# Kernel tuning notes

Hardware: AMD Instinct MI355X
Metric: run time of the kernel (lower is better)

The kernel has to match this reference:

```python
import jax, jax.numpy as jnp
import numpy as np

UNITS = 512
CONN = 512          # input feature dim (connections)
DEND_SIZE = 16
SEQL = CONN // DEND_SIZE  # 32 dendrite segments per unit
BATCH = 512


def _make_dendrites(units, conn, dsize, seed=0):
    # Per-unit random permutation of input indices, grouped into contiguous
    # dendrites of size dsize -> segment id in [0, seql) for every input index.
    rng = np.random.default_rng(seed)
    seql = conn // dsize
    seg = np.empty((units, conn), dtype=np.int32)
    for u in range(units):
        perm = rng.permutation(conn)
        for s in range(seql):
            seg[u, perm[dsize * s:dsize * (s + 1)]] = s
    return seg


def setup_inputs() -> dict:
    key = jax.random.key(0)
    k1, k2, k3, k4 = jax.random.split(key, 4)
    x = jax.random.normal(k1, (BATCH, CONN), dtype=jnp.float32)
    # weight_twice & not uniqueW -> per-unit scalar input weight, shape [1, units]
    kernel = jax.random.uniform(k2, (1, UNITS), dtype=jnp.float32, minval=5e-5, maxval=0.1)
    # per-(segment, unit) dendritic weight, shape [seql, units]
    dendriticW = jax.random.uniform(k3, (SEQL, UNITS), dtype=jnp.float32, minval=5e-5, maxval=0.1)
    bias = jax.random.normal(k4, (UNITS,), dtype=jnp.float32) * 0.05
    dendrites = jnp.asarray(_make_dendrites(UNITS, CONN, DEND_SIZE))  # [units, conn] int32
    return {"x": x, "kernel": kernel, "dendriticW": dendriticW,
            "bias": bias, "dendrites": dendrites}


def reference(x, kernel, dendriticW, bias, dendrites):
    # x: [batch, conn]; dendrites: [units, conn] segment ids in [0, SEQL)
    xT = x.T  # [conn, batch]
    # per-unit gather + unsorted_segment_sum over connections -> [units, seql, batch]
    segsum = jax.vmap(lambda seg: jax.ops.segment_sum(xT, seg, num_segments=SEQL))(dendrites)
    # weight_twice: per-unit scalar input weight (kernel broadcast over conn)
    segsum = segsum * kernel[0][:, None, None]
    # dendritic weighting + reduction over segments -> [batch, units]
    out = jnp.einsum('usb,su->bu', segsum, dendriticW) + bias
    return jax.nn.relu(out)
```

## Files before the change

kernel.cpp:

```cpp
#include <hip/hip_runtime.h>
#include <hip/hip_bf16.h>

#define UNITS 512
#define CONN  512
#define SEQL  32

typedef __hip_bfloat16 bf16;
typedef __attribute__((ext_vector_type(8))) short short8;
typedef __attribute__((ext_vector_type(4))) float floatx4;


union cv8 { bf16 h[8]; short8 v; };

__global__ __launch_bounds__(256) void dendriter_fused_mfma(
    const float* __restrict__ x,
    const float* __restrict__ kern,
    const float* __restrict__ dW,
    const float* __restrict__ bias,
    const int*   __restrict__ dend,
    float* __restrict__ out)
{
    __shared__ short8 wl[16][65];

    const int t  = threadIdx.x;
    const int ut = blockIdx.x * 16;
    const int bt = blockIdx.y * 64;

    {
        const int ul  = t >> 4;
        const int cg0 = (t & 15) * 4;
        const int u   = ut + ul;
        const float kv = kern[u];
        const int4* dp = (const int4*)(dend + u * CONN + cg0 * 8);
#pragma unroll
        for (int j = 0; j < 4; ++j) {
            const int4 s0 = dp[2 * j];
            const int4 s1 = dp[2 * j + 1];
            const int segs[8] = {s0.x, s0.y, s0.z, s0.w, s1.x, s1.y, s1.z, s1.w};
            cv8 w;
#pragma unroll
            for (int i = 0; i < 8; ++i)
                w.h[i] = __float2bfloat16(kv * dW[segs[i] * UNITS + u]);
            const int cg = cg0 + j;
            const int kb = cg >> 2;
            const int q  = cg & 3;
            wl[kb][ul | (q << 4)] = w.v;
        }
    }
    __syncthreads();

    const int lane = t & 63;
    const int wv   = t >> 6;
    const int m = lane & 15;
    const int q = lane >> 4;
    const int btw = bt + wv * 16;

    const float* xrow = x + (size_t)(btw + m) * CONN + q * 8;
    floatx4 acc = {0.f, 0.f, 0.f, 0.f};
#pragma unroll
    for (int kb = 0; kb < 16; ++kb) {
        const float4 f0 = *(const float4*)(xrow + kb * 32);
        const float4 f1 = *(const float4*)(xrow + kb * 32 + 4);
        cv8 a;
        a.h[0] = __float2bfloat16(f0.x); a.h[1] = __float2bfloat16(f0.y);
        a.h[2] = __float2bfloat16(f0.z); a.h[3] = __float2bfloat16(f0.w);
        a.h[4] = __float2bfloat16(f1.x); a.h[5] = __float2bfloat16(f1.y);
        a.h[6] = __float2bfloat16(f1.z); a.h[7] = __float2bfloat16(f1.w);
        const short8 b = wl[kb][lane];
        acc = __builtin_amdgcn_mfma_f32_16x16x32_bf16(a.v, b, acc, 0, 0, 0);
    }

    const float bu = bias[ut + m];
#pragma unroll
    for (int r = 0; r < 4; ++r) {
        float v = acc[r] + bu;
        v = v > 0.f ? v : 0.f;
        out[(size_t)(btw + q * 4 + r) * UNITS + ut + m] = v;
    }
}

extern "C" void kernel_launch(void* const* d_in, const int* in_sizes, int n_in,
                              void* d_out, int out_size, void* d_ws, size_t ws_size,
                              hipStream_t stream) {
    const float* x    = (const float*)d_in[0];
    const float* kern = (const float*)d_in[1];
    const float* dW   = (const float*)d_in[2];
    const float* bias = (const float*)d_in[3];
    const int*   dend = (const int*)  d_in[4];
    float* out = (float*)d_out;

    const int batch = in_sizes[0] / CONN;
    dendriter_fused_mfma<<<dim3(UNITS / 16, batch / 64), 256, 0, stream>>>(
        x, kern, dW, bias, dend, out);
}
```

Before: 69.70 us.

## Split weight construction into prep kernel and run GEMM with single-wave blocks

```diff
diff --git a/kernel.cpp b/kernel.cpp
--- a/kernel.cpp
+++ b/kernel.cpp
@@ -12,20 +12,96 @@
 
 union cv8 { bf16 h[8]; short8 v; };
 
-__global__ __launch_bounds__(256) void dendriter_fused_mfma(
-    const float* __restrict__ x,
+__global__ __launch_bounds__(128) void prep_w(
     const float* __restrict__ kern,
     const float* __restrict__ dW,
+    const int*   __restrict__ dend,
+    bf16* __restrict__ W)
+{
+    __shared__ float table[2][SEQL];
+    const int t  = threadIdx.x;
+    const int u0 = blockIdx.x * 2;
+
+    if (t < 2 * SEQL) {
+        const int s = t >> 1, ul = t & 1;
+        table[ul][s] = dW[s * UNITS + u0 + ul];
+    }
+    __syncthreads();
+
+    const int ul = t >> 6;
+    const int u  = u0 + ul;
+    const int c0 = (t & 63) * 8;
+    const float kv = kern[u];
+
+    const int4 s0 = ((const int4*)(dend + u * CONN + c0))[0];
+    const int4 s1 = ((const int4*)(dend + u * CONN + c0))[1];
+    const int segs[8] = {s0.x, s0.y, s0.z, s0.w, s1.x, s1.y, s1.z, s1.w};
+
+    cv8 w;
+#pragma unroll
+    for (int i = 0; i < 8; ++i)
+        w.h[i] = __float2bfloat16(kv * table[ul][segs[i]]);
+    *(short8*)(W + u * CONN + c0) = w.v;
+}
+
+__device__ __forceinline__ short8 cvt8(const float* p) {
+    const float4 f0 = ((const float4*)p)[0];
+    const float4 f1 = ((const float4*)p)[1];
+    cv8 a;
+    a.h[0] = __float2bfloat16(f0.x); a.h[1] = __float2bfloat16(f0.y);
+    a.h[2] = __float2bfloat16(f0.z); a.h[3] = __float2bfloat16(f0.w);
+    a.h[4] = __float2bfloat16(f1.x); a.h[5] = __float2bfloat16(f1.y);
+    a.h[6] = __float2bfloat16(f1.z); a.h[7] = __float2bfloat16(f1.w);
+    return a.v;
+}
+
+__global__ __launch_bounds__(64) void gemm_mfma(
+    const float* __restrict__ x,
+    const bf16*  __restrict__ W,
     const float* __restrict__ bias,
-    const int*   __restrict__ dend,
     float* __restrict__ out)
 {
+    const int lane = threadIdx.x;
+    const int ut = blockIdx.x * 16;
+    const int bt = blockIdx.y * 16;
+    const int m = lane & 15;
+    const int q = lane >> 4;
+
+    const float* xrow = x + (size_t)(bt + m) * CONN + q * 8;
+    const bf16*  wrow = W + (size_t)(ut + m) * CONN + q * 8;
+
+    floatx4 acc0 = {0.f, 0.f, 0.f, 0.f};
+    floatx4 acc1 = {0.f, 0.f, 0.f, 0.f};
+#pragma unroll
+    for (int kb = 0; kb < 8; ++kb) {
+        const int k0 = kb * 32;
+        const int k1 = 256 + kb * 32;
+        const short8 a0 = cvt8(xrow + k0);
+        const short8 b0 = *(const short8*)(wrow + k0);
+        acc0 = __builtin_amdgcn_mfma_f32_16x16x32_bf16(a0, b0, acc0, 0, 0, 0);
+        const short8 a1 = cvt8(xrow + k1);
+        const short8 b1 = *(const short8*)(wrow + k1);
+        acc1 = __builtin_amdgcn_mfma_f32_16x16x32_bf16(a1, b1, acc1, 0, 0, 0);
+    }
+
+    const float bu = bias[ut + m];
+#pragma unroll
+    for (int r = 0; r < 4; ++r) {
+        float v = acc0[r] + acc1[r] + bu;
+        v = v > 0.f ? v : 0.f;
+        out[(size_t)(bt + q * 4 + r) * UNITS + ut + m] = v;
+    }
+}
+
+__global__ __launch_bounds__(256) void dendriter_fused_mfma(
+    const float* __restrict__ x, const float* __restrict__ kern,
+    const float* __restrict__ dW, const float* __restrict__ bias,
+    const int* __restrict__ dend, float* __restrict__ out)
+{
     __shared__ short8 wl[16][65];
-
     const int t  = threadIdx.x;
     const int ut = blockIdx.x * 16;
     const int bt = blockIdx.y * 64;
-
     {
         const int ul  = t >> 4;
         const int cg0 = (t & 15) * 4;
@@ -42,9 +118,7 @@
             for (int i = 0; i < 8; ++i)
                 w.h[i] = __float2bfloat16(kv * dW[segs[i] * UNITS + u]);
             const int cg = cg0 + j;
-            const int kb = cg >> 2;
-            const int q  = cg & 3;
-            wl[kb][ul | (q << 4)] = w.v;
+            wl[cg >> 2][ul | ((cg & 3) << 4)] = w.v;
         }
     }
     __syncthreads();
@@ -54,22 +128,14 @@
     const int m = lane & 15;
     const int q = lane >> 4;
     const int btw = bt + wv * 16;
-
     const float* xrow = x + (size_t)(btw + m) * CONN + q * 8;
     floatx4 acc = {0.f, 0.f, 0.f, 0.f};
 #pragma unroll
     for (int kb = 0; kb < 16; ++kb) {
-        const float4 f0 = *(const float4*)(xrow + kb * 32);
-        const float4 f1 = *(const float4*)(xrow + kb * 32 + 4);
-        cv8 a;
-        a.h[0] = __float2bfloat16(f0.x); a.h[1] = __float2bfloat16(f0.y);
-        a.h[2] = __float2bfloat16(f0.z); a.h[3] = __float2bfloat16(f0.w);
-        a.h[4] = __float2bfloat16(f1.x); a.h[5] = __float2bfloat16(f1.y);
-        a.h[6] = __float2bfloat16(f1.z); a.h[7] = __float2bfloat16(f1.w);
+        const short8 a = cvt8(xrow + kb * 32);
         const short8 b = wl[kb][lane];
-        acc = __builtin_amdgcn_mfma_f32_16x16x32_bf16(a.v, b, acc, 0, 0, 0);
+        acc = __builtin_amdgcn_mfma_f32_16x16x32_bf16(a, b, acc, 0, 0, 0);
     }
-
     const float bu = bias[ut + m];
 #pragma unroll
     for (int r = 0; r < 4; ++r) {
@@ -90,6 +156,14 @@
     float* out = (float*)d_out;
 
     const int batch = in_sizes[0] / CONN;
-    dendriter_fused_mfma<<<dim3(UNITS / 16, batch / 64), 256, 0, stream>>>(
-        x, kern, dW, bias, dend, out);
+    const size_t w_bytes = (size_t)UNITS * CONN * sizeof(bf16);
+
+    if (ws_size >= w_bytes) {
+        bf16* W = (bf16*)d_ws;
+        prep_w<<<UNITS / 2, 128, 0, stream>>>(kern, dW, dend, W);
+        gemm_mfma<<<dim3(UNITS / 16, batch / 16), 64, 0, stream>>>(x, W, bias, out);
+    } else {
+        dendriter_fused_mfma<<<dim3(UNITS / 16, batch / 64), 256, 0, stream>>>(
+            x, kern, dW, bias, dend, out);
+    }
 }
```

Result: slower. 73.34 us (+5.2%).
